# Kernel tuning notes

Hardware: AMD Instinct MI355X
Metric: run time of the kernel (lower is better)

## Reference

```python
import jax, jax.numpy as jnp
import numpy as np

B, S, D, H, HD = 2, 2048, 2048, 16, 128  # batch, seq, embed, heads, head_dim


def setup_inputs() -> dict:
    key = jax.random.key(0)
    k0, k1, k2 = jax.random.split(key, 3)
    hidden_states = jax.random.normal(k0, (B, S, D), dtype=jnp.float32)
    # fused QKV projection: [D, H*HD + 2*HD] (multi-query: single shared K and V head)
    W_attn = jax.random.normal(k1, (D, H * HD + 2 * HD), dtype=jnp.float32) * 0.02
    b_attn = jnp.zeros((H * HD + 2 * HD,), dtype=jnp.float32)
    W_proj = jax.random.normal(k2, (D, D), dtype=jnp.float32) * 0.02
    b_proj = jnp.zeros((D,), dtype=jnp.float32)
    # causal mask, broadcastable to (B, Q, H, K); True = attend
    attention_mask = jnp.tril(jnp.ones((S, S), dtype=bool))[None, :, None, :]
    return {
        "hidden_states": hidden_states,
        "W_attn": W_attn,
        "b_attn": b_attn,
        "W_proj": W_proj,
        "b_proj": b_proj,
        "attention_mask": attention_mask,
    }


def reference(hidden_states, W_attn, b_attn, W_proj, b_proj, attention_mask):
    # fused QKV, then split into Q (H heads) and shared K/V (multi-query)
    qkv = hidden_states @ W_attn + b_attn          # (B, S, H*HD + 2*HD)
    q = qkv[..., : H * HD].reshape(B, S, H, HD)    # (B, Q, H, hd)
    key_t = qkv[..., H * HD : H * HD + HD]         # (B, K, hd) shared K head
    value = qkv[..., H * HD + HD :]                # (B, K, hd) shared V head

    # dtype == softmax_dtype (fp32) -> upcast=False, unscale=1
    scale_factor = 1.0 / (HD ** 0.5)               # scale_attn_weights
    attn_weights = jnp.einsum("bqhd,bkd->bqhk", q, key_t) * scale_factor
    mask_value = jnp.finfo(jnp.float32).min
    attn_weights = jnp.where(attention_mask, attn_weights, mask_value)
    attn_weights = jax.nn.softmax(attn_weights, axis=-1)

    attn_output = jnp.einsum("bqhk,bkd->bqhd", attn_weights, value)
    attn_output = attn_output.reshape(B, S, H * HD)
    return attn_output @ W_proj + b_proj           # (B, S, D)
```

## Files before the change

kernel.cpp:

```cpp
#include <hip/hip_runtime.h>
#include <math.h>

constexpr int cB  = 2;
constexpr int cS  = 2048;
constexpr int cD  = 2048;
constexpr int cH  = 16;
constexpr int cHD = 128;
constexpr int cNQKV = cH * cHD + 2 * cHD;

typedef __attribute__((ext_vector_type(8))) short bf16x8;
typedef __attribute__((ext_vector_type(4))) float f32x4;
typedef __attribute__((ext_vector_type(16))) float f32x16;

__device__ __forceinline__ short f2bf(float f) {
    union { float f; unsigned u; } v; v.f = f;
    unsigned r = (v.u + 0x7FFFu + ((v.u >> 16) & 1u)) >> 16;
    return (short)r;
}

__device__ __forceinline__ unsigned pk_bf16(float lo, float hi_) {
    return (unsigned)(unsigned short)f2bf(lo)
         | ((unsigned)(unsigned short)f2bf(hi_) << 16);
}

typedef __attribute__((address_space(3))) void lds_t;
typedef const __attribute__((address_space(1))) void gbl_t;
__device__ __forceinline__ void gld16(const void* g, void* l) {
    __builtin_amdgcn_global_load_lds((gbl_t*)g, (lds_t*)l, 16, 0, 0);
}

__global__ __launch_bounds__(256) void conv_bf16(
    const float* __restrict__ src, short* __restrict__ dst)
{
    size_t i = ((size_t)blockIdx.x * 256 + threadIdx.x) * 8;
    float4 a = *(const float4*)(src + i);
    float4 b = *(const float4*)(src + i + 4);
    bf16x8 o;
    o[0] = f2bf(a.x); o[1] = f2bf(a.y); o[2] = f2bf(a.z); o[3] = f2bf(a.w);
    o[4] = f2bf(b.x); o[5] = f2bf(b.y); o[6] = f2bf(b.z); o[7] = f2bf(b.w);
    *(bf16x8*)(dst + i) = o;
}

__global__ __launch_bounds__(256) void transpose_bf16(
    const float* __restrict__ src, short* __restrict__ dst, int K, int N)
{
    __shared__ short t[32][33];
    const int n0 = blockIdx.x * 32, k0 = blockIdx.y * 32;
    const int x = threadIdx.x & 31, y = threadIdx.x >> 5;
#pragma unroll
    for (int i = 0; i < 4; ++i)
        t[y + 8 * i][x] = f2bf(src[(size_t)(k0 + y + 8 * i) * N + n0 + x]);
    __syncthreads();
#pragma unroll
    for (int i = 0; i < 4; ++i)
        dst[(size_t)(n0 + y + 8 * i) * K + k0 + x] = t[x][y + 8 * i];
}

template<bool BF16_OUT>
__global__ __launch_bounds__(256) void gemm_mfma(
    const short* __restrict__ A, const short* __restrict__ Bt,
    const float* __restrict__ bias, void* __restrict__ Cout,
    int M, int N, int K, float qscale, int qcols)
{
    __shared__ short As[128 * 32];
    __shared__ short Bs[128 * 32];

    const int tid = threadIdx.x;
    const int lane = tid & 63, n16 = lane & 15, quad = lane >> 4;
    const int wave = tid >> 6, wm = wave >> 1, wn = wave & 1;
    const int m0 = blockIdx.y * 128, n0 = blockIdx.x * 128;

    f32x4 acc[4][4];
#pragma unroll
    for (int i = 0; i < 4; ++i)
#pragma unroll
        for (int j = 0; j < 4; ++j) acc[i][j] = 0.0f;

    const int s0 = tid, s1 = tid + 256;
    const short* Ag0 = A  + (size_t)(m0 + (s0 >> 2)) * K + (s0 & 3) * 8;
    const short* Ag1 = A  + (size_t)(m0 + (s1 >> 2)) * K + (s1 & 3) * 8;
    const short* Bg0 = Bt + (size_t)(n0 + (s0 >> 2)) * K + (s0 & 3) * 8;
    const short* Bg1 = Bt + (size_t)(n0 + (s1 >> 2)) * K + (s1 & 3) * 8;

    for (int k0 = 0; k0 < K; k0 += 32) {
        gld16(Ag0 + k0, &As[s0 * 8]);
        gld16(Ag1 + k0, &As[s1 * 8]);
        gld16(Bg0 + k0, &Bs[s0 * 8]);
        gld16(Bg1 + k0, &Bs[s1 * 8]);
        __syncthreads();
        bf16x8 af[4], bfr[4];
#pragma unroll
        for (int mt = 0; mt < 4; ++mt)
            af[mt] = *(const bf16x8*)&As[(wm * 64 + mt * 16 + n16) * 32 + quad * 8];
#pragma unroll
        for (int nt = 0; nt < 4; ++nt)
            bfr[nt] = *(const bf16x8*)&Bs[(wn * 64 + nt * 16 + n16) * 32 + quad * 8];
#pragma unroll
        for (int mt = 0; mt < 4; ++mt)
#pragma unroll
            for (int nt = 0; nt < 4; ++nt)
                acc[mt][nt] = __builtin_amdgcn_mfma_f32_16x16x32_bf16(
                    af[mt], bfr[nt], acc[mt][nt], 0, 0, 0);
        __syncthreads();
    }

#pragma unroll
    for (int nt = 0; nt < 4; ++nt) {
        const int col = n0 + wn * 64 + nt * 16 + n16;
        const float bv = bias[col];
        const float sc = (col < qcols) ? qscale : 1.0f;
#pragma unroll
        for (int mt = 0; mt < 4; ++mt)
#pragma unroll
            for (int r = 0; r < 4; ++r) {
                const int row = m0 + wm * 64 + mt * 16 + quad * 4 + r;
                const float v = (acc[mt][nt][r] + bv) * sc;
                if (BF16_OUT) ((short*)Cout)[(size_t)row * N + col] = f2bf(v);
                else          ((float*)Cout)[(size_t)row * N + col] = v;
            }
    }
}

__global__ __launch_bounds__(256) void prep_v(
    const short* __restrict__ qkvb, short* __restrict__ Vt)
{
    const int b  = blockIdx.y;
    const int k0 = blockIdx.x * 64;
    const int t  = threadIdx.x;
#pragma unroll
    for (int i = 0; i < 32; ++i) {
        int idx = i * 256 + t;
        int hd = idx >> 6, key = idx & 63;
        Vt[((size_t)b * cHD + hd) * cS + k0 + key] =
            qkvb[((size_t)(b * cS + k0 + key)) * cNQKV + cH * cHD + cHD + hd];
    }
}

__global__ __launch_bounds__(256, 2) void attn_mfma(
    const short* __restrict__ qkvb, const short* __restrict__ Vt,
    short* __restrict__ out)
{
    const int tid  = threadIdx.x;
    const int wave = tid >> 6;
    const int lane = tid & 63;
    const int q32  = lane & 31;
    const int hi   = lane >> 5;
    const int qhalf = wave & 1;
    const int khalf = wave >> 1;
    const int h  = blockIdx.y;
    const int b  = blockIdx.z;

    __shared__ __align__(16) short Ks[2][64 * 128];
    __shared__ __align__(16) short Vs[2][128 * 64];
    __shared__ __align__(16) float Linv[2][32];
    float* Obuf = (float*)Ks;
    float* Lbuf = (float*)Vs;

    const short* kglob = qkvb + (size_t)b * cS * cNQKV + cH * cHD;
    const short* vbase = Vt + (size_t)b * cHD * cS;

    const int kl = lane >> 4;
    const int kx = (lane & 15) * 16;
    const int vdl = lane >> 3;
    const int vx  = (lane & 7) * 16;

    int cur = 0;

    auto stage = [&](int buf, int k0) {
#pragma unroll
        for (int j = 0; j < 4; ++j) {
            const int i = wave * 4 + j;
            const int keyt = i * 4 + kl;
            const int srcb = kx ^ ((keyt & 15) << 4);
            gld16((const char*)(kglob + (size_t)(k0 + keyt) * cNQKV) + srcb,
                  &Ks[buf][i * 512]);
        }
#pragma unroll
        for (int j = 0; j < 4; ++j) {
            const int i = wave * 4 + j;
            const int d = i * 8 + vdl;
            const int srcb = vx ^ ((d & 7) << 4);
            gld16((const char*)(vbase + (size_t)d * cS + k0) + srcb,
                  &Vs[buf][i * 512]);
        }
    };

#pragma unroll 1
    for (int seg = 0; seg < 2; ++seg) {
        const int qt = seg ? (int)blockIdx.x : 31 - (int)blockIdx.x;
        const int qb = qt * 64;
        const int qg = qb + qhalf * 32 + q32;
        const int nkt = qt + 1;

        bf16x8 qf[8];
        {
            const short* qbase = qkvb + ((size_t)(b * cS) + qg) * cNQKV
                               + h * cHD + hi * 8;
#pragma unroll
            for (int dblk = 0; dblk < 8; ++dblk)
                qf[dblk] = *(const bf16x8*)(qbase + dblk * 16);
        }

        f32x16 oc[4];
#pragma unroll
        for (int i = 0; i < 4; ++i) oc[i] = 0.0f;
        float lp = 0.0f;

        __syncthreads();
        stage(cur, 0);

#pragma unroll 1
        for (int kt = 0; kt < nkt; ++kt) {
            const int k0 = kt * 64;
            __syncthreads();
            if (kt + 1 < nkt) stage(cur ^ 1, k0 + 64);

            f32x16 sc = 0.0f;
            {
                const int key = khalf * 32 + q32;
                const char* krow = (const char*)&Ks[cur][key * 128];
                const int swz = (key & 15) << 4;
                __builtin_amdgcn_s_setprio(1);
#pragma unroll
                for (int dblk = 0; dblk < 8; ++dblk) {
                    bf16x8 kf = *(const bf16x8*)(krow + ((dblk * 32 + hi * 16) ^ swz));
                    sc = __builtin_amdgcn_mfma_f32_32x32x16_bf16(
                        kf, qf[dblk], sc, 0, 0, 0);
                }
                __builtin_amdgcn_s_setprio(0);
            }

            const bool diag = (kt == nkt - 1);
            float e[16];
#pragma unroll
            for (int r = 0; r < 16; ++r) {
                float s = sc[r];
                if (diag) {
                    int kgl = k0 + khalf * 32 + (r & 3) + 8 * (r >> 2) + 4 * hi;
                    if (kgl > qg) s = -1e30f;
                }
                float p = __expf(s);
                lp += p;
                e[r] = p;
            }

            bf16x8 pa[2];
#pragma unroll
            for (int kblk = 0; kblk < 2; ++kblk) {
                const int rb = 8 * kblk;
                unsigned wA0 = pk_bf16(e[rb + 0], e[rb + 1]);
                unsigned wA1 = pk_bf16(e[rb + 2], e[rb + 3]);
                unsigned wB0 = pk_bf16(e[rb + 4], e[rb + 5]);
                unsigned wB1 = pk_bf16(e[rb + 6], e[rb + 7]);
                unsigned keep0 = hi ? wB0 : wA0, keep1 = hi ? wB1 : wA1;
                unsigned send0 = hi ? wA0 : wB0, send1 = hi ? wA1 : wB1;
                unsigned recv0 = (unsigned)__shfl_xor((int)send0, 32);
                unsigned recv1 = (unsigned)__shfl_xor((int)send1, 32);
                union { unsigned u[4]; bf16x8 v; } uu;
                uu.u[0] = hi ? recv0 : keep0;
                uu.u[1] = hi ? recv1 : keep1;
                uu.u[2] = hi ? keep0 : recv0;
                uu.u[3] = hi ? keep1 : recv1;
                pa[kblk] = uu.v;
            }

            __builtin_amdgcn_s_setprio(1);
#pragma unroll
            for (int kblk = 0; kblk < 2; ++kblk)
#pragma unroll
                for (int dtile = 0; dtile < 4; ++dtile) {
                    const int d = dtile * 32 + q32;
                    const char* vrow = (const char*)&Vs[cur][d * 64];
                    bf16x8 vf = *(const bf16x8*)(vrow +
                        ((khalf * 64 + kblk * 32 + hi * 16) ^ ((d & 7) << 4)));
                    oc[dtile] = __builtin_amdgcn_mfma_f32_32x32x16_bf16(
                        pa[kblk], vf, oc[dtile], 0, 0, 0);
                }
            __builtin_amdgcn_s_setprio(0);

            cur ^= 1;
        }

        lp += __shfl_xor(lp, 32);
        __syncthreads();
        if (khalf == 1) {
            float* ob = Obuf + qhalf * 32 * 128;
#pragma unroll
            for (int dtile = 0; dtile < 4; ++dtile)
#pragma unroll
                for (int r = 0; r < 16; ++r) {
                    const int q = (r & 3) + 8 * (r >> 2) + 4 * hi;
                    ob[q * 128 + dtile * 32 + q32] = oc[dtile][r];
                }
            if (hi == 0) Lbuf[qhalf * 32 + q32] = lp;
        }
        __syncthreads();
        if (khalf == 0) {
            float* ob = Obuf + qhalf * 32 * 128;
#pragma unroll
            for (int dtile = 0; dtile < 4; ++dtile)
#pragma unroll
                for (int r = 0; r < 16; ++r) {
                    const int q = (r & 3) + 8 * (r >> 2) + 4 * hi;
                    oc[dtile][r] += ob[q * 128 + dtile * 32 + q32];
                }
            lp += Lbuf[qhalf * 32 + q32];
            if (hi == 0) Linv[qhalf][q32] = 1.0f / lp;
        }
        __syncthreads();
        if (khalf == 0) {
            f32x4 invv[4];
#pragma unroll
            for (int g = 0; g < 4; ++g)
                invv[g] = *(const f32x4*)&Linv[qhalf][g * 8 + hi * 4];
            short* obase = out + ((size_t)(b * cS) + qb + qhalf * 32) * cD + h * cHD;
#pragma unroll
            for (int dtile = 0; dtile < 4; ++dtile)
#pragma unroll
                for (int r = 0; r < 16; ++r) {
                    const int q = (r & 3) + 8 * (r >> 2) + 4 * hi;
                    obase[(size_t)q * cD + dtile * 32 + q32] =
                        f2bf(oc[dtile][r] * invv[r >> 2][r & 3]);
                }
        }
    }
}

extern "C" void kernel_launch(void* const* d_in, const int* in_sizes, int n_in,
                              void* d_out, int out_size, void* d_ws, size_t ws_size,
                              hipStream_t stream)
{
    const float* hidden = (const float*)d_in[0];
    const float* W_attn = (const float*)d_in[1];
    const float* b_attn = (const float*)d_in[2];
    const float* W_proj = (const float*)d_in[3];
    const float* b_proj = (const float*)d_in[4];
    float* out = (float*)d_out;

    const int M = cB * cS;
    short* qkvb = (short*)d_ws;
    short* Ah   = qkvb + (size_t)M * cNQKV;
    short* Wb   = Ah   + (size_t)M * cD;
    short* Wpb  = Wb   + (size_t)cNQKV * cD;
    short* Vt   = Wpb  + (size_t)cD * cD;
    short* attno = Ah;

    const float scale = 0.088388347648318447f;

    conv_bf16<<<(size_t)M * cD / 2048, 256, 0, stream>>>(hidden, Ah);
    transpose_bf16<<<dim3(cNQKV / 32, cD / 32), 256, 0, stream>>>(W_attn, Wb, cD, cNQKV);
    transpose_bf16<<<dim3(cD / 32, cD / 32), 256, 0, stream>>>(W_proj, Wpb, cD, cD);

    gemm_mfma<true><<<dim3(cNQKV / 128, M / 128), 256, 0, stream>>>(
        Ah, Wb, b_attn, qkvb, M, cNQKV, cD, scale, cH * cHD);

    prep_v<<<dim3(cS / 64, cB), 256, 0, stream>>>(qkvb, Vt);

    attn_mfma<<<dim3(16, cH, cB), 256, 0, stream>>>(qkvb, Vt, attno);

    gemm_mfma<false><<<dim3(cD / 128, M / 128), 256, 0, stream>>>(
        attno, Wpb, b_proj, out, M, cD, cD, 1.0f, 0);
}
```

Baseline: 336.5 us.

## Load K and V fragments directly from global memory instead of LDS staging

```diff
diff --git a/kernel.cpp b/kernel.cpp
--- a/kernel.cpp
+++ b/kernel.cpp
@@ -150,40 +150,12 @@
     const int h  = blockIdx.y;
     const int b  = blockIdx.z;
 
-    __shared__ __align__(16) short Ks[2][64 * 128];
-    __shared__ __align__(16) short Vs[2][128 * 64];
-    __shared__ __align__(16) float Linv[2][32];
-    float* Obuf = (float*)Ks;
-    float* Lbuf = (float*)Vs;
+    __shared__ __align__(16) float Obuf[2][32][128];
+    __shared__ float Lbuf[2][32];
+    __shared__ float Linv[2][32];
 
     const short* kglob = qkvb + (size_t)b * cS * cNQKV + cH * cHD;
     const short* vbase = Vt + (size_t)b * cHD * cS;
-
-    const int kl = lane >> 4;
-    const int kx = (lane & 15) * 16;
-    const int vdl = lane >> 3;
-    const int vx  = (lane & 7) * 16;
-
-    int cur = 0;
-
-    auto stage = [&](int buf, int k0) {
-#pragma unroll
-        for (int j = 0; j < 4; ++j) {
-            const int i = wave * 4 + j;
-            const int keyt = i * 4 + kl;
-            const int srcb = kx ^ ((keyt & 15) << 4);
-            gld16((const char*)(kglob + (size_t)(k0 + keyt) * cNQKV) + srcb,
-                  &Ks[buf][i * 512]);
-        }
-#pragma unroll
-        for (int j = 0; j < 4; ++j) {
-            const int i = wave * 4 + j;
-            const int d = i * 8 + vdl;
-            const int srcb = vx ^ ((d & 7) << 4);
-            gld16((const char*)(vbase + (size_t)d * cS + k0) + srcb,
-                  &Vs[buf][i * 512]);
-        }
-    };
 
 #pragma unroll 1
     for (int seg = 0; seg < 2; ++seg) {
@@ -206,28 +178,30 @@
         for (int i = 0; i < 4; ++i) oc[i] = 0.0f;
         float lp = 0.0f;
 
-        __syncthreads();
-        stage(cur, 0);
+        const short* krbase = kglob + (size_t)(khalf * 32 + q32) * cNQKV + hi * 8;
+
+        bf16x8 kfc[8];
+#pragma unroll
+        for (int dblk = 0; dblk < 8; ++dblk)
+            kfc[dblk] = *(const bf16x8*)(krbase + dblk * 16);
 
 #pragma unroll 1
         for (int kt = 0; kt < nkt; ++kt) {
             const int k0 = kt * 64;
-            __syncthreads();
-            if (kt + 1 < nkt) stage(cur ^ 1, k0 + 64);
 
             f32x16 sc = 0.0f;
-            {
-                const int key = khalf * 32 + q32;
-                const char* krow = (const char*)&Ks[cur][key * 128];
-                const int swz = (key & 15) << 4;
-                __builtin_amdgcn_s_setprio(1);
-#pragma unroll
-                for (int dblk = 0; dblk < 8; ++dblk) {
-                    bf16x8 kf = *(const bf16x8*)(krow + ((dblk * 32 + hi * 16) ^ swz));
-                    sc = __builtin_amdgcn_mfma_f32_32x32x16_bf16(
-                        kf, qf[dblk], sc, 0, 0, 0);
-                }
-                __builtin_amdgcn_s_setprio(0);
+            __builtin_amdgcn_s_setprio(1);
+#pragma unroll
+            for (int dblk = 0; dblk < 8; ++dblk)
+                sc = __builtin_amdgcn_mfma_f32_32x32x16_bf16(
+                    kfc[dblk], qf[dblk], sc, 0, 0, 0);
+            __builtin_amdgcn_s_setprio(0);
+
+            if (kt + 1 < nkt) {
+                const short* krn = krbase + (size_t)(k0 + 64) * cNQKV;
+#pragma unroll
+                for (int dblk = 0; dblk < 8; ++dblk)
+                    kfc[dblk] = *(const bf16x8*)(krn + dblk * 16);
             }
 
             const bool diag = (kt == nkt - 1);
@@ -242,6 +216,15 @@
                 float p = __expf(s);
                 lp += p;
                 e[r] = p;
+            }
+
+            bf16x8 vf0[4], vf1[4];
+#pragma unroll
+            for (int dtile = 0; dtile < 4; ++dtile) {
+                const short* vr = vbase + (size_t)(dtile * 32 + q32) * cS
+                                + k0 + khalf * 32 + hi * 8;
+                vf0[dtile] = *(const bf16x8*)(vr);
+                vf1[dtile] = *(const bf16x8*)(vr + 16);
             }
 
             bf16x8 pa[2];
@@ -266,25 +249,19 @@
 
             __builtin_amdgcn_s_setprio(1);
 #pragma unroll
-            for (int kblk = 0; kblk < 2; ++kblk)
-#pragma unroll
-                for (int dtile = 0; dtile < 4; ++dtile) {
-                    const int d = dtile * 32 + q32;
-                    const char* vrow = (const char*)&Vs[cur][d * 64];
-                    bf16x8 vf = *(const bf16x8*)(vrow +
-                        ((khalf * 64 + kblk * 32 + hi * 16) ^ ((d & 7) << 4)));
-                    oc[dtile] = __builtin_amdgcn_mfma_f32_32x32x16_bf16(
-                        pa[kblk], vf, oc[dtile], 0, 0, 0);
-                }
+            for (int dtile = 0; dtile < 4; ++dtile) {
+                oc[dtile] = __builtin_amdgcn_mfma_f32_32x32x16_bf16(
+                    pa[0], vf0[dtile], oc[dtile], 0, 0, 0);
+                oc[dtile] = __builtin_amdgcn_mfma_f32_32x32x16_bf16(
+                    pa[1], vf1[dtile], oc[dtile], 0, 0, 0);
+            }
             __builtin_amdgcn_s_setprio(0);
-
-            cur ^= 1;
         }
 
         lp += __shfl_xor(lp, 32);
         __syncthreads();
         if (khalf == 1) {
-            float* ob = Obuf + qhalf * 32 * 128;
+            float* ob = &Obuf[qhalf][0][0];
 #pragma unroll
             for (int dtile = 0; dtile < 4; ++dtile)
 #pragma unroll
@@ -292,11 +269,11 @@
                     const int q = (r & 3) + 8 * (r >> 2) + 4 * hi;
                     ob[q * 128 + dtile * 32 + q32] = oc[dtile][r];
                 }
-            if (hi == 0) Lbuf[qhalf * 32 + q32] = lp;
+            if (hi == 0) Lbuf[qhalf][q32] = lp;
         }
         __syncthreads();
         if (khalf == 0) {
-            float* ob = Obuf + qhalf * 32 * 128;
+            const float* ob = &Obuf[qhalf][0][0];
 #pragma unroll
             for (int dtile = 0; dtile < 4; ++dtile)
 #pragma unroll
@@ -304,7 +281,7 @@
                     const int q = (r & 3) + 8 * (r >> 2) + 4 * hi;
                     oc[dtile][r] += ob[q * 128 + dtile * 32 + q32];
                 }
-            lp += Lbuf[qhalf * 32 + q32];
+            lp += Lbuf[qhalf][q32];
             if (hi == 0) Linv[qhalf][q32] = 1.0f / lp;
         }
         __syncthreads();
```

After: 385.8 us. +14.7%, slower.
